# Optimization experiments

Measured on AMD Instinct MI355X. Metric: run time of the kernel, lower is better.

## Reference

```python
import jax, jax.numpy as jnp
import numpy as np

N_TOPICS = 1024
TOPIC_DIM = 128
HIDDEN = 512
N_HEADS = 8
HEAD_DIM = HIDDEN // N_HEADS
N_LAYERS = 2
ALPHA = 0.2
TIME_DECAY = 0.1
BATCH = 8


def setup_inputs() -> dict:
    key = jax.random.key(0)
    ks = jax.random.split(key, 16)
    inp = {
        'topic_ids': jax.random.randint(ks[0], (BATCH,), 0, N_TOPICS, dtype=jnp.int32),
        'adj_matrix': jax.random.randint(ks[1], (BATCH, N_TOPICS, N_TOPICS), 0, 2, dtype=jnp.int32),
        'time_matrix': jax.random.uniform(ks[2], (BATCH, N_TOPICS, N_TOPICS), dtype=jnp.float32),
        'attractiveness': jax.random.normal(ks[3], (BATCH,), dtype=jnp.float32),
        # parameters (torch Linear convention: W [out,in], y = x@W.T + b)
        'topic_embedding': jax.random.normal(ks[4], (N_TOPICS, TOPIC_DIM), dtype=jnp.float32) * 0.1,
        'struct_W': jax.random.normal(ks[5], (HIDDEN, TOPIC_DIM), dtype=jnp.float32) * 0.05,
        'struct_b': jnp.zeros((HIDDEN,), dtype=jnp.float32),
        'attract_W': jax.random.normal(ks[6], (HIDDEN, 1), dtype=jnp.float32) * 0.05,
        'attract_b': jnp.zeros((HIDDEN,), dtype=jnp.float32),
        'gat_W': jax.random.normal(ks[7], (N_LAYERS, N_HEADS, HIDDEN, HEAD_DIM), dtype=jnp.float32) * 0.05,
        'gat_a': jax.random.normal(ks[8], (N_LAYERS, N_HEADS, 2 * HEAD_DIM, 1), dtype=jnp.float32) * 0.05,
        'fc1_W': jax.random.normal(ks[9], (HIDDEN, HIDDEN), dtype=jnp.float32) * 0.05,
        'fc1_b': jnp.zeros((HIDDEN,), dtype=jnp.float32),
        'fc2_W': jax.random.normal(ks[10], (1, HIDDEN), dtype=jnp.float32) * 0.05,
        'fc2_b': jnp.zeros((1,), dtype=jnp.float32),
    }
    return inp


def _gat_layer(node, adj, time_w, W, a):
    # node: [B,N,F], adj: [B,N,N] (0/1), time_w: [B,N,N]
    # W: [H,F,hd], a: [H,2*hd,1]
    h = jnp.einsum('bni,hio->bhno', node, W)  # [B,H,N,hd]
    # Additive attention: a = [a_src; a_dst] so e_ij = LeakyReLU(h_i.a_src + h_j.a_dst)
    a_src = a[:, :HEAD_DIM, 0]   # [H,hd]
    a_dst = a[:, HEAD_DIM:, 0]   # [H,hd]
    e_src = jnp.einsum('bhnd,hd->bhn', h, a_src)  # [B,H,N]
    e_dst = jnp.einsum('bhnd,hd->bhn', h, a_dst)  # [B,H,N]
    e = e_src[:, :, :, None] + e_dst[:, :, None, :]  # [B,H,N,N]
    e = jax.nn.leaky_relu(e, negative_slope=ALPHA)
    e = e * time_w[:, None, :, :]
    e = jnp.where(adj[:, None, :, :] == 0, -jnp.inf, e)
    attn = jax.nn.softmax(e, axis=-1)
    out = jnp.einsum('bhij,bhjd->bhid', attn, h)  # [B,H,N,hd]
    out = out.transpose(0, 2, 1, 3).reshape(node.shape[0], node.shape[1], -1)
    return jax.nn.elu(out)


def reference(topic_ids, adj_matrix, time_matrix, attractiveness,
              topic_embedding, struct_W, struct_b, attract_W, attract_b,
              gat_W, gat_a, fc1_W, fc1_b, fc2_W, fc2_b):
    # structural features for all topics -> hidden
    struct = topic_embedding @ struct_W.T + struct_b          # [N,hidden]
    attract = attractiveness[:, None] @ attract_W.T + attract_b  # [B,hidden]
    node = jnp.broadcast_to(struct[None], (BATCH, N_TOPICS, HIDDEN))
    # weighted co-occurrence time (eq.17)
    time_w = jnp.exp(-TIME_DECAY * (time_matrix.max() - time_matrix))  # [B,N,N]
    for l in range(N_LAYERS):
        node = _gat_layer(node, adj_matrix, time_w, gat_W[l], gat_a[l])
    # gather per-sample topic node feature
    topic_feat = jnp.take_along_axis(node, topic_ids[:, None, None].astype(jnp.int32), axis=1)[:, 0]  # [B,hidden]
    combined = topic_feat + attract
    hidden = jax.nn.relu(combined @ fc1_W.T + fc1_b)
    pred = hidden @ fc2_W.T + fc2_b  # [B,1]
    return pred
```

## Files before the change

kernel.cpp:

```cpp
#include <hip/hip_runtime.h>

#define NT 1024
#define TD 128
#define HID 512
#define NH 8
#define HD 64
#define NB 8

typedef unsigned short us;
typedef short bf16x8 __attribute__((ext_vector_type(8)));
typedef float f32x4 __attribute__((ext_vector_type(4)));

#define LOG2E 1.44269504f

__device__ __forceinline__ us f2bf(float x) {
    unsigned int u = __float_as_uint(x);
    return (us)((u + 0x7FFFu + ((u >> 16) & 1u)) >> 16);
}
__device__ __forceinline__ float bf2f(us s) {
    return __uint_as_float(((unsigned int)s) << 16);
}

__global__ __launch_bounds__(256) void kprep(const float* __restrict__ tm, float* __restrict__ part,
                                             const float* __restrict__ emb, const float* __restrict__ sW,
// ... 18 lines not shown
    } else if (bx < 1152) {
        int g = bx - 1024; int iblk = g & 15, oseg = g >> 4;
        us* As = (us*)smf;
        us* Bs = (us*)smf + 64 * 136;
        const float4* esrc = (const float4*)(emb + (size_t)iblk * 64 * TD);
        const float4* wsrc = (const float4*)(sW + (size_t)oseg * 64 * TD);
        #pragma unroll
        for (int rep = 0; rep < 8; rep++) {
            int f = rep * 256 + t;
            int row = f >> 5, c4 = f & 31;
            float4 av = esrc[f];
            float4 bv = wsrc[f];
            us pa[4] = {f2bf(av.x), f2bf(av.y), f2bf(av.z), f2bf(av.w)};
            us pb[4] = {f2bf(bv.x), f2bf(bv.y), f2bf(bv.z), f2bf(bv.w)};
            *(uint2*)&As[row * 136 + c4 * 4] = *(uint2*)pa;
            *(uint2*)&Bs[row * 136 + c4 * 4] = *(uint2*)pb;
        }
        __syncthreads();
        int l = t & 63, w = t >> 6, m = l & 15, q = l >> 4;
        f32x4 acc[4];
        #pragma unroll
        for (int ot = 0; ot < 4; ot++) acc[ot] = (f32x4){0.f, 0.f, 0.f, 0.f};
        #pragma unroll
        for (int ks = 0; ks < 4; ks++) {
            bf16x8 a = *(const bf16x8*)&As[(w * 16 + m) * 136 + ks * 32 + q * 8];
            #pragma unroll
            for (int ot = 0; ot < 4; ot++) {
                bf16x8 b = *(const bf16x8*)&Bs[(ot * 16 + m) * 136 + ks * 32 + q * 8];
                acc[ot] = __builtin_amdgcn_mfma_f32_16x16x32_bf16(a, b, acc[ot], 0, 0, 0);
            }
        }
        #pragma unroll
        for (int ot = 0; ot < 4; ot++) {
            int col = oseg * 64 + ot * 16 + m;
            float sbv = sb[col];
            #pragma unroll
            for (int rr = 0; rr < 4; rr++) {
                int rowi = iblk * 64 + w * 16 + q * 4 + rr;
                node0b[(size_t)rowi * HID + col] = f2bf(acc[ot][rr] + sbv);
            }
        }
    } else if (bx < 1280) {
        int g = bx - 1152; int lh = g >> 3, kt = g & 7;
        float* tile = smf;
        const float4* src = (const float4*)(gW + ((size_t)lh * HID + kt * 64) * HD);
        #pragma unroll
        for (int rep = 0; rep < 4; rep++) {
            int f = rep * 256 + t;
            float4 v = src[f];
            int row = f >> 4, col = (f & 15) * 4;
            float* d = tile + row * 65 + col;
            d[0] = v.x; d[1] = v.y; d[2] = v.z; d[3] = v.w;
        }
        __syncthreads();
        int o = t >> 2, ks = (t & 3) * 16;
        us pk[16];
        #pragma unroll
        for (int j = 0; j < 16; j++) pk[j] = f2bf(tile[(ks + j) * 65 + o]);
        us* dst = Wt + (size_t)lh * HD * HID + (size_t)o * HID + kt * 64 + ks;
        *(uint4*)dst = *(uint4*)pk;
        *(uint4*)(dst + 8) = *(uint4*)&pk[8];
    } else {
        int hp = bx - 1280;
        if (hp == 0 && t < NB) out[t] = fc2b[0];
        const float* gsrc = ga + (size_t)(NH + hp) * 2 * HD;
        const float* wbase = gW + (size_t)(NH + hp) * HID * HD;
        #pragma unroll
        for (int rep = 0; rep < 2; rep++) {
            int k = rep * 256 + t;
            const float* wr = wbase + (size_t)k * HD;
            float s = 0.f, d = 0.f;
            #pragma unroll 8
            for (int o = 0; o < HD; o++) {
                float wv = wr[o];
                s = fmaf(wv, gsrc[o], s);
                d = fmaf(wv, gsrc[HD + o], d);
            }
            ws2[hp * HID + k] = s;
            ws2[(8 + hp) * HID + k] = d;
        }
    }
}

__device__ __forceinline__ void gemm_body(const us* __restrict__ A, const us* __restrict__ W,
                                          const float* __restrict__ gav,
                                          us* __restrict__ outT,
                                          float* __restrict__ esO, float* __restrict__ edO,
                                          int iblk, int b, int h, int t, us* sm) {
    us* As = sm;
    us* Bs = sm + 2 * 4608;
    int row = t >> 2, ks = t & 3;
    int l = t & 63, w = t >> 6, m = l & 15, q = l >> 4;
    size_t arow0 = (size_t)(b * NT + iblk * 64);
    const us* ar = A + (arow0 + row) * HID + ks * 16;
    const us* br = W + ((size_t)(h * HD + row)) * HID + ks * 16;
    f32x4 acc[4];
    #pragma unroll
    for (int ot = 0; ot < 4; ot++) acc[ot] = (f32x4){0.f, 0.f, 0.f, 0.f};
    {
        uint4 x0 = *(const uint4*)ar, x1 = *(const uint4*)(ar + 8);
        uint4 y0 = *(const uint4*)br, y1 = *(const uint4*)(br + 8);
        *(uint4*)&As[row * 72 + ks * 16] = x0; *(uint4*)&As[row * 72 + ks * 16 + 8] = x1;
        *(uint4*)&Bs[row * 72 + ks * 16] = y0; *(uint4*)&Bs[row * 72 + ks * 16 + 8] = y1;
    }
    uint4 a0 = *(const uint4*)(ar + 64), a1 = *(const uint4*)(ar + 72);
    uint4 b0 = *(const uint4*)(br + 64), b1 = *(const uint4*)(br + 72);
    for (int it = 0; it < 8; it++) {
        int cur = it & 1, nxt = cur ^ 1;
        uint4 na0, na1, nb0, nb1;
        if (it < 6) {
            int k0 = (it + 2) * 64;
            na0 = *(const uint4*)(ar + k0); na1 = *(const uint4*)(ar + k0 + 8);
            nb0 = *(const uint4*)(br + k0); nb1 = *(const uint4*)(br + k0 + 8);
        }
        __syncthreads();
        if (it < 7) {
            *(uint4*)&As[nxt * 4608 + row * 72 + ks * 16] = a0;
            *(uint4*)&As[nxt * 4608 + row * 72 + ks * 16 + 8] = a1;
            *(uint4*)&Bs[nxt * 4608 + row * 72 + ks * 16] = b0;
            *(uint4*)&Bs[nxt * 4608 + row * 72 + ks * 16 + 8] = b1;
        }
        const us* Ac = As + cur * 4608; const us* Bc = Bs + cur * 4608;
        #pragma unroll
        for (int kt = 0; kt < 2; kt++) {
            bf16x8 av = *(const bf16x8*)&Ac[(w * 16 + m) * 72 + kt * 32 + q * 8];
            #pragma unroll
            for (int ot = 0; ot < 4; ot++) {
                bf16x8 bv = *(const bf16x8*)&Bc[(ot * 16 + m) * 72 + kt * 32 + q * 8];
                acc[ot] = __builtin_amdgcn_mfma_f32_16x16x32_bf16(av, bv, acc[ot], 0, 0, 0);
            }
        }
        if (it < 6) { a0 = na0; a1 = na1; b0 = nb0; b1 = nb1; }
    }
    const float* gas = gav + h * 2 * HD;
    float gs[4], gd[4];
    #pragma unroll
    for (int ot = 0; ot < 4; ot++) { gs[ot] = gas[ot * 16 + m]; gd[ot] = gas[HD + ot * 16 + m]; }
    size_t ebase = ((size_t)b * NH + h) * NT + iblk * 64;
    #pragma unroll
    for (int rr = 0; rr < 4; rr++) {
        float s = 0.f, d = 0.f;
        #pragma unroll
        for (int ot = 0; ot < 4; ot++) { float v = acc[ot][rr]; s = fmaf(v, gs[ot], s); d = fmaf(v, gd[ot], d); }
        #pragma unroll
        for (int mask = 1; mask < 16; mask <<= 1) { s += __shfl_xor(s, mask); d += __shfl_xor(d, mask); }
        if (m == 0) {
            int rowi = w * 16 + q * 4 + rr;
            esO[ebase + rowi] = s;
            edO[ebase + rowi] = d;
        }
    }
    #pragma unroll
    for (int ot = 0; ot < 4; ot++) {
        int col = h * HD + ot * 16 + m;
        #pragma unroll
        for (int rr = 0; rr < 4; rr++) {
            int i_loc = w * 16 + q * 4 + rr;
            outT[(size_t)col * NT + iblk * 64 + i_loc] = f2bf(acc[ot][rr]);
        }
    }
}

#define ZF4 33808
__global__ __launch_bounds__(256) void kphase1(const float* __restrict__ tm, const int* __restrict__ adj,
                                               const float* __restrict__ part, us* __restrict__ TWb,
                                               const us* __restrict__ node0b, const us* __restrict__ Wt,
                                               const float* __restrict__ ga, us* __restrict__ Ht1,
                                               float* __restrict__ es1, float* __restrict__ ed1,
                                               float* __restrict__ zbase) {
    __shared__ __align__(16) us sm[4 * 4608];
    int bx = blockIdx.x, t = threadIdx.x;
    if (bx < 2048) {
        float* red = (float*)sm;
        float m = fmaxf(fmaxf(part[t * 4], part[t * 4 + 1]), fmaxf(part[t * 4 + 2], part[t * 4 + 3]));
        red[t] = m; __syncthreads();
        for (int s = 128; s > 0; s >>= 1) { if (t < s) red[t] = fmaxf(red[t], red[t + s]); __syncthreads(); }
        float tmx = red[0];
        const float C = 0.1f * LOG2E;
        #pragma unroll
        for (int it = 0; it < 4; it++) {
            size_t idx = (((size_t)bx * 4 + it) * 256 + t) * 4;
            float4 tv = *(const float4*)(tm + idx);
            int4 av = *(const int4*)(adj + idx);
            float w0 = exp2f((tv.x - tmx) * C) * LOG2E;
            float w1 = exp2f((tv.y - tmx) * C) * LOG2E;
            float w2 = exp2f((tv.z - tmx) * C) * LOG2E;
            float w3 = exp2f((tv.w - tmx) * C) * LOG2E;
            unsigned int fa = av.x ? __float_as_uint(w0) : 0x7FC00000u;
            unsigned int fb = av.y ? __float_as_uint(w1) : 0x7FC00000u;
            unsigned int fc = av.z ? __float_as_uint(w2) : 0x7FC00000u;
            unsigned int fd = av.w ? __float_as_uint(w3) : 0x7FC00000u;
            uint2 pk;
            pk.x = __builtin_amdgcn_perm(fb, fa, 0x07060302);
            pk.y = __builtin_amdgcn_perm(fd, fc, 0x07060302);
            *(uint2*)&TWb[idx] = pk;
        }
    } else if (bx < 2176) {
        int g = bx - 2048;
        gemm_body(node0b, Wt, ga, Ht1, es1, ed1, g & 15, 0, g >> 4, t, sm);
    } else {
        size_t idx = (size_t)(bx - 2176) * 256 + t;
        if (idx < ZF4) ((float4*)zbase)[idx] = (float4){0.f, 0.f, 0.f, 0.f};
    }
}

__global__ __launch_bounds__(256) void kedge(const float* __restrict__ es, const float* __restrict__ ed,
                                             us* __restrict__ E1) {
    int g = blockIdx.x;
    int h = g >> 8, i0 = (g & 255) << 2;
    int t = threadIdx.x;
    __shared__ float eds[NT];
    *(float4*)&eds[t * 4] = *(const float4*)&ed[h * NT + t * 4];
    __syncthreads();
    int j = t * 4;
    float4 e4 = *(const float4*)&eds[j];
    #pragma unroll
    for (int r = 0; r < 4; r++) {
        float esv = es[h * NT + i0 + r];
        float a = esv + e4.x; a = fmaxf(a, 0.2f * a);
        float bq = esv + e4.y; bq = fmaxf(bq, 0.2f * bq);
        float c = esv + e4.z; c = fmaxf(c, 0.2f * c);
        float d = esv + e4.w; d = fmaxf(d, 0.2f * d);
        uint2 pk;
        pk.x = __builtin_amdgcn_perm(__float_as_uint(bq), __float_as_uint(a), 0x07060302);
        pk.y = __builtin_amdgcn_perm(__float_as_uint(d), __float_as_uint(c), 0x07060302);
        *(uint2*)&E1[((size_t)(h * NT) + i0 + r) * NT + j] = pk;
    }
}

__device__ __forceinline__ void compute_p(uint4 T0, uint4 T1, uint4 E0, uint4 E1v,
                                          uint4& P01, uint4& P23) {
    union U { uint4 v; unsigned int w[4]; };
    U t0; t0.v = T0; U t1; t1.v = T1; U e0; e0.v = E0; U e1; e1.v = E1v;
    unsigned int pk[8];
    #pragma unroll
    for (int r = 0; r < 4; r++) {
        float twa = __uint_as_float(t0.w[r] << 16);
        float twb = __uint_as_float(t0.w[r] & 0xFFFF0000u);
        float Ea  = __uint_as_float(e0.w[r] << 16);
        float Eb  = __uint_as_float(e0.w[r] & 0xFFFF0000u);
        float pa = fmaxf(exp2f(twa * Ea), 0.f);
        float pb = fmaxf(exp2f(twb * Eb), 0.f);
        pk[r] = __builtin_amdgcn_perm(__float_as_uint(pb), __float_as_uint(pa), 0x07060302);
    }
    #pragma unroll
    for (int r = 0; r < 4; r++) {
        float twa = __uint_as_float(t1.w[r] << 16);
        float twb = __uint_as_float(t1.w[r] & 0xFFFF0000u);
        float Ea  = __uint_as_float(e1.w[r] << 16);
        float Eb  = __uint_as_float(e1.w[r] & 0xFFFF0000u);
        float pa = fmaxf(exp2f(twa * Ea), 0.f);
        float pb = fmaxf(exp2f(twb * Eb), 0.f);
        pk[4 + r] = __builtin_amdgcn_perm(__float_as_uint(pb), __float_as_uint(pa), 0x07060302);
    }
    P01 = make_uint4(pk[0], pk[1], pk[2], pk[3]);
    P23 = make_uint4(pk[4], pk[5], pk[6], pk[7]);
}

__global__ __launch_bounds__(256) void kattn1(const us* __restrict__ TWb, const us* __restrict__ Ht,
                                              const us* __restrict__ E1, const float* __restrict__ ws2,
                                              us* __restrict__ node1b,
                                              float* __restrict__ es2, float* __restrict__ ed2) {
    int x = blockIdx.x; int iblk = x & 15; int b = x >> 4; int h = blockIdx.y;
    int t = threadIdx.x;
    __shared__ __align__(16) us Ps[2 * 4608];
    __shared__ __align__(16) us Hs[2 * 4608];
    __shared__ float invl_s[64];
    int i = t >> 2, js = t & 3;
    int l = t & 63, w = t >> 6, m = l & 15, q = l >> 4;
    const us* twrow = TWb + ((size_t)(b * NT) + iblk * 64 + i) * NT + js * 16;
    const us* erow  = E1 + ((size_t)(h * NT) + iblk * 64 + i) * NT + js * 16;
    const us* htrow = Ht + ((size_t)(h * HD) + i) * NT + js * 16;
    f32x4 acc[4];
    #pragma unroll
    for (int ot = 0; ot < 4; ot++) acc[ot] = (f32x4){0.f, 0.f, 0.f, 0.f};
    f32x4 acc1 = (f32x4){0.f, 0.f, 0.f, 0.f};
    short ov = (m == 0) ? (short)0x3F80 : (short)0;
    bf16x8 bones = {ov, ov, ov, ov, ov, ov, ov, ov};
    uint4 T0, T1, E0, E1r, Hh0, Hh1;
    T0 = *(const uint4*)twrow; T1 = *(const uint4*)(twrow + 8);
    E0 = *(const uint4*)erow;  E1r = *(const uint4*)(erow + 8);
    Hh0 = *(const uint4*)htrow; Hh1 = *(const uint4*)(htrow + 8);
    {
        uint4 p01, p23;
        compute_p(T0, T1, E0, E1r, p01, p23);
        us* Pd = Ps + i * 72 + js * 16;
        us* Hd = Hs + i * 72 + js * 16;
        *(uint4*)Pd = p01; *(uint4*)(Pd + 8) = p23;
        *(uint4*)Hd = Hh0; *(uint4*)(Hd + 8) = Hh1;
    }
    T0 = *(const uint4*)(twrow + 64); T1 = *(const uint4*)(twrow + 72);
    E0 = *(const uint4*)(erow + 64);  E1r = *(const uint4*)(erow + 72);
    Hh0 = *(const uint4*)(htrow + 64); Hh1 = *(const uint4*)(htrow + 72);
    for (int it = 0; it < 16; it++) {
        int cur = it & 1, nxt = cur ^ 1;
        uint4 nT0, nT1, nE0, nE1, nH0, nH1;
        if (it < 14) {
            int j0 = (it + 2) * 64;
            nT0 = *(const uint4*)(twrow + j0); nT1 = *(const uint4*)(twrow + j0 + 8);
            nE0 = *(const uint4*)(erow + j0);  nE1 = *(const uint4*)(erow + j0 + 8);
            nH0 = *(const uint4*)(htrow + j0); nH1 = *(const uint4*)(htrow + j0 + 8);
        }
        uint4 p01, p23;
        if (it < 15) compute_p(T0, T1, E0, E1r, p01, p23);
        __syncthreads();
        if (it < 15) {
            us* Pd = Ps + nxt * 4608 + i * 72 + js * 16;
            us* Hd = Hs + nxt * 4608 + i * 72 + js * 16;
            *(uint4*)Pd = p01; *(uint4*)(Pd + 8) = p23;
            *(uint4*)Hd = Hh0; *(uint4*)(Hd + 8) = Hh1;
        }
        const us* Pc = Ps + cur * 4608; const us* Hc = Hs + cur * 4608;
        #pragma unroll
        for (int kt = 0; kt < 2; kt++) {
            bf16x8 av = *(const bf16x8*)&Pc[(w * 16 + m) * 72 + kt * 32 + q * 8];
            #pragma unroll
            for (int ot = 0; ot < 4; ot++) {
                bf16x8 bv = *(const bf16x8*)&Hc[(ot * 16 + m) * 72 + kt * 32 + q * 8];
                acc[ot] = __builtin_amdgcn_mfma_f32_16x16x32_bf16(av, bv, acc[ot], 0, 0, 0);
            }
            acc1 = __builtin_amdgcn_mfma_f32_16x16x32_bf16(av, bones, acc1, 0, 0, 0);
        }
        if (it < 14) { T0 = nT0; T1 = nT1; E0 = nE0; E1r = nE1; Hh0 = nH0; Hh1 = nH1; }
    }
    if (m == 0) {
        #pragma unroll
        for (int rr = 0; rr < 4; rr++) invl_s[w * 16 + q * 4 + rr] = 1.f / acc1[rr];
    }
    __syncthreads();
    float varr[4][4];
    #pragma unroll
    for (int ot = 0; ot < 4; ot++) {
        int col = h * HD + ot * 16 + m;
        #pragma unroll
        for (int rr = 0; rr < 4; rr++) {
            int i_loc = w * 16 + q * 4 + rr;
            float v = acc[ot][rr] * invl_s[i_loc];
            v = v > 0.f ? v : (__expf(v) - 1.f);
            varr[ot][rr] = v;
            node1b[(size_t)(b * NT + iblk * 64 + i_loc) * HID + col] = f2bf(v);
        }
    }
    #pragma unroll
    for (int h2 = 0; h2 < NH; h2++) {
        float wsv[4], wdv[4];
        #pragma unroll
        for (int ot = 0; ot < 4; ot++) {
            int col = h * HD + ot * 16 + m;
            wsv[ot] = ws2[h2 * HID + col];
            wdv[ot] = ws2[(8 + h2) * HID + col];
        }
        #pragma unroll
        for (int rr = 0; rr < 4; rr++) {
            float s = 0.f, d = 0.f;
            #pragma unroll
            for (int ot = 0; ot < 4; ot++) { s = fmaf(varr[ot][rr], wsv[ot], s); d = fmaf(varr[ot][rr], wdv[ot], d); }
            #pragma unroll
            for (int mask = 1; mask < 16; mask <<= 1) { s += __shfl_xor(s, mask); d += __shfl_xor(d, mask); }
            if (m == 0) {
                int ig = iblk * 64 + w * 16 + q * 4 + rr;
                atomicAdd(&es2[(size_t)(b * NH + h2) * NT + ig], s);
                atomicAdd(&ed2[(size_t)(b * NH + h2) * NT + ig], d);
            }
        }
    }
}

__global__ __launch_bounds__(256) void kgemm2(const us* __restrict__ node1b, const us* __restrict__ Wt2,
                                              const us* __restrict__ TWb,
                                              const float* __restrict__ es2, const float* __restrict__ ed2,
                                              const int* __restrict__ topic_ids,
                                              float* __restrict__ pv, float* __restrict__ pl) {
    __shared__ __align__(16) us sm[4 * 4608];
    __shared__ float pv_s[4][64];
    __shared__ float pl_s[4];
    int x = blockIdx.x; int iblk = x & 15; int b = x >> 4; int h = blockIdx.y;
    int t = threadIdx.x;
    us* As = sm;
    us* Bs = sm + 2 * 4608;
    int row = t >> 2, ks = t & 3;
    int l = t & 63, w = t >> 6, m = l & 15, q = l >> 4;
    size_t arow0 = (size_t)(b * NT + iblk * 64);
    const us* ar = node1b + (arow0 + row) * HID + ks * 16;
    const us* br = Wt2 + ((size_t)(h * HD + row)) * HID + ks * 16;
    f32x4 acc[4];
    #pragma unroll
    for (int ot = 0; ot < 4; ot++) acc[ot] = (f32x4){0.f, 0.f, 0.f, 0.f};
    {
        uint4 x0 = *(const uint4*)ar, x1 = *(const uint4*)(ar + 8);
        uint4 y0 = *(const uint4*)br, y1 = *(const uint4*)(br + 8);
        *(uint4*)&As[row * 72 + ks * 16] = x0; *(uint4*)&As[row * 72 + ks * 16 + 8] = x1;
        *(uint4*)&Bs[row * 72 + ks * 16] = y0; *(uint4*)&Bs[row * 72 + ks * 16 + 8] = y1;
    }
    uint4 a0 = *(const uint4*)(ar + 64), a1 = *(const uint4*)(ar + 72);
    uint4 b0 = *(const uint4*)(br + 64), b1 = *(const uint4*)(br + 72);
    for (int it = 0; it < 8; it++) {
        int cur = it & 1, nxt = cur ^ 1;
        uint4 na0, na1, nb0, nb1;
        if (it < 6) {
            int k0 = (it + 2) * 64;
            na0 = *(const uint4*)(ar + k0); na1 = *(const uint4*)(ar + k0 + 8);
            nb0 = *(const uint4*)(br + k0); nb1 = *(const uint4*)(br + k0 + 8);
        }
        __syncthreads();
        if (it < 7) {
            *(uint4*)&As[nxt * 4608 + row * 72 + ks * 16] = a0;
            *(uint4*)&As[nxt * 4608 + row * 72 + ks * 16 + 8] = a1;
            *(uint4*)&Bs[nxt * 4608 + row * 72 + ks * 16] = b0;
            *(uint4*)&Bs[nxt * 4608 + row * 72 + ks * 16 + 8] = b1;
        }
        const us* Ac = As + cur * 4608; const us* Bc = Bs + cur * 4608;
        #pragma unroll
        for (int kt = 0; kt < 2; kt++) {
            bf16x8 av = *(const bf16x8*)&Ac[(w * 16 + m) * 72 + kt * 32 + q * 8];
            #pragma unroll
            for (int ot = 0; ot < 4; ot++) {
                bf16x8 bv = *(const bf16x8*)&Bc[(ot * 16 + m) * 72 + kt * 32 + q * 8];
                acc[ot] = __builtin_amdgcn_mfma_f32_16x16x32_bf16(av, bv, acc[ot], 0, 0, 0);
            }
        }
        if (it < 6) { a0 = na0; a1 = na1; b0 = nb0; b1 = nb1; }
    }
    int qi = topic_ids[b];
    float es_q = es2[(size_t)(b * NH + h) * NT + qi];
    float pvp[4] = {0.f, 0.f, 0.f, 0.f};
    float psum = 0.f;
    #pragma unroll
    for (int rr = 0; rr < 4; rr++) {
        int j = iblk * 64 + w * 16 + q * 4 + rr;
        float edj = ed2[(size_t)(b * NH + h) * NT + j];
        float tw = bf2f(TWb[((size_t)(b * NT) + qi) * NT + j]);
        float e = es_q + edj;
        e = fmaxf(e, 0.2f * e) * tw;
        float pj = fmaxf(exp2f(e), 0.f);
        psum += pj;
        #pragma unroll
        for (int ot = 0; ot < 4; ot++) pvp[ot] = fmaf(pj, acc[ot][rr], pvp[ot]);
    }
    #pragma unroll
    for (int mask = 16; mask < 64; mask <<= 1) {
        psum += __shfl_xor(psum, mask);
        #pragma unroll
        for (int ot = 0; ot < 4; ot++) pvp[ot] += __shfl_xor(pvp[ot], mask);
    }
    if (q == 0) {
        #pragma unroll
        for (int ot = 0; ot < 4; ot++) pv_s[w][ot * 16 + m] = pvp[ot];
        if (m == 0) pl_s[w] = psum;
    }
    __syncthreads();
    if (t < 64) {
        float s = pv_s[0][t] + pv_s[1][t] + pv_s[2][t] + pv_s[3][t];
        atomicAdd(&pv[(size_t)(b * NH + h) * HD + t], s);
    }
    if (t == 0) atomicAdd(&pl[b * NH + h], pl_s[0] + pl_s[1] + pl_s[2] + pl_s[3]);
}

__global__ __launch_bounds__(256) void khead2(const float* __restrict__ pv, const float* __restrict__ pl,
                                              const float* __restrict__ attr,
                                              const float* __restrict__ aW, const float* __restrict__ ab,
                                              const float* __restrict__ fc1W, const float* __restrict__ fc1b,
                                              const float* __restrict__ fc2W, float* __restrict__ out) {
    int kseg = blockIdx.x, b = blockIdx.y;
    int t = threadIdx.x;
    __shared__ float comb[HID];
    __shared__ float linv[NH];
    __shared__ float r2[256];
    if (t < NH) linv[t] = 1.f / pl[b * NH + t];
    __syncthreads();
    float av = attr[b];
    for (int k = t; k < HID; k += 256) {
        int h = k >> 6, o = k & 63;
        float v = pv[(size_t)(b * NH + h) * HD + o] * linv[h];
        v = v > 0.f ? v : (__expf(v) - 1.f);
        comb[k] = v + av * aW[k] + ab[k];
    }
    __syncthreads();
    int kk = kseg * 16 + (t >> 4);
    int j = t & 15;
    const float* row = fc1W + (size_t)kk * HID;
    float acc = 0.f;
    #pragma unroll 8
    for (int mi = 0; mi < 32; mi++) {
        int idx = mi * 16 + j;
        acc = fmaf(comb[idx], row[idx], acc);
    }
    #pragma unroll
    for (int mask = 1; mask < 16; mask <<= 1) acc += __shfl_xor(acc, mask);
    float partv = 0.f;
    if (j == 0) {
        float hk = fmaxf(acc + fc1b[kk], 0.f);
        partv = hk * fc2W[kk];
    }
    r2[t] = partv; __syncthreads();
    for (int s = 128; s > 0; s >>= 1) { if (t < s) r2[t] += r2[t + s]; __syncthreads(); }
    if (t == 0) atomicAdd(&out[b], r2[0]);
}

extern "C" void kernel_launch(void* const* d_in, const int* in_sizes, int n_in,
                              void* d_out, int out_size, void* d_ws, size_t ws_size,
                              hipStream_t stream) {
    const int*   topic_ids = (const int*)d_in[0];
    const int*   adj       = (const int*)d_in[1];
    const float* tm        = (const float*)d_in[2];
    const float* attr      = (const float*)d_in[3];
    const float* emb       = (const float*)d_in[4];
    const float* sW        = (const float*)d_in[5];
    const float* sb        = (const float*)d_in[6];
    const float* aW        = (const float*)d_in[7];
    const float* ab        = (const float*)d_in[8];
    const float* gW        = (const float*)d_in[9];
    const float* ga        = (const float*)d_in[10];
    const float* fc1W      = (const float*)d_in[11];
    const float* fc1b      = (const float*)d_in[12];
    const float* fc2W      = (const float*)d_in[13];
    const float* fc2b      = (const float*)d_in[14];
    float* out = (float*)d_out;

    char* p = (char*)d_ws;
    us* TWb    = (us*)p; p += sizeof(us) * (size_t)NB * NT * NT;
    us* E1     = (us*)p; p += sizeof(us) * (size_t)NH * NT * NT;
    us* node0b = (us*)p; p += sizeof(us) * (size_t)NT * HID;
    us* Wt     = (us*)p; p += sizeof(us) * (size_t)2 * NH * HD * HID;
    us* Ht1    = (us*)p; p += sizeof(us) * (size_t)HID * NT;
    us* node1b = (us*)p; p += sizeof(us) * (size_t)NB * NT * HID;
    float* es1  = (float*)p; p += sizeof(float) * NH * NT;
    float* ed1  = (float*)p; p += sizeof(float) * NH * NT;
    float* es2  = (float*)p; p += sizeof(float) * NB * NH * NT;
    float* ed2  = (float*)p; p += sizeof(float) * NB * NH * NT;
    float* pv   = (float*)p; p += sizeof(float) * NB * NH * HD;
    float* pl   = (float*)p; p += sizeof(float) * NB * NH;
    float* ws2  = (float*)p; p += sizeof(float) * 16 * HID;
    float* part = (float*)p; p += sizeof(float) * 1024;

    kprep<<<1288, 256, 0, stream>>>(tm, part, emb, sW, sb, node0b, gW, Wt, ga, ws2, fc2b, out);
    kphase1<<<2309, 256, 0, stream>>>(tm, adj, part, TWb, node0b, Wt, ga, Ht1, es1, ed1, es2);
    kedge<<<2048, 256, 0, stream>>>(es1, ed1, E1);
    kattn1<<<dim3(16 * NB, NH), 256, 0, stream>>>(TWb, Ht1, E1, ws2, node1b, es2, ed2);
    kgemm2<<<dim3(16 * NB, NH), 256, 0, stream>>>(node1b, Wt + (size_t)NH * HD * HID, TWb,
                                                  es2, ed2, topic_ids, pv, pl);
    khead2<<<dim3(32, NB), 256, 0, stream>>>(pv, pl, attr, aW, ab, fc1W, fc1b, fc2W, out);
}
```

Baseline: 211.9 us.

## Drop LDS staging in GEMMs and compute only query-row layer-2 scores

The three MFMA loops (layer-1 projection, attention aggregation, layer-2 projection) now load operands straight from global memory into registers in the MFMA fragment layout. This removes the shared-memory double buffers and barriers. Layer-2 source scores are now computed only for the queried topic row, and destination scores are computed inline in kgemm2 from its accumulators. That removes the full es2/ed2 buffers, their per-row atomic updates and the large zero-fill. The cost is less reuse of global loads within a block, so more traffic goes through L2, and unaligned 16-byte row loads may coalesce less well.

```diff
diff --git a/kernel.cpp b/kernel.cpp
--- a/kernel.cpp
+++ b/kernel.cpp
@@ -124,61 +124,28 @@
     }
 }
 
-__device__ __forceinline__ void gemm_body(const us* __restrict__ A, const us* __restrict__ W,
-                                          const float* __restrict__ gav,
-                                          us* __restrict__ outT,
-                                          float* __restrict__ esO, float* __restrict__ edO,
-                                          int iblk, int b, int h, int t, us* sm) {
-    us* As = sm;
-    us* Bs = sm + 2 * 4608;
-    int row = t >> 2, ks = t & 3;
+__device__ __forceinline__ void gemm1_body(const us* __restrict__ A, const us* __restrict__ W,
+                                           const float* __restrict__ gav, us* __restrict__ outT,
+                                           float* __restrict__ esO, float* __restrict__ edO,
+                                           int iblk, int h, int t) {
     int l = t & 63, w = t >> 6, m = l & 15, q = l >> 4;
-    size_t arow0 = (size_t)(b * NT + iblk * 64);
-    const us* ar = A + (arow0 + row) * HID + ks * 16;
-    const us* br = W + ((size_t)(h * HD + row)) * HID + ks * 16;
+    const us* ar = A + ((size_t)(iblk * 64 + w * 16 + m)) * HID + q * 8;
+    const us* br = W + ((size_t)(h * HD) + m) * HID + q * 8;
     f32x4 acc[4];
     #pragma unroll
     for (int ot = 0; ot < 4; ot++) acc[ot] = (f32x4){0.f, 0.f, 0.f, 0.f};
-    {
-        uint4 x0 = *(const uint4*)ar, x1 = *(const uint4*)(ar + 8);
-        uint4 y0 = *(const uint4*)br, y1 = *(const uint4*)(br + 8);
-        *(uint4*)&As[row * 72 + ks * 16] = x0; *(uint4*)&As[row * 72 + ks * 16 + 8] = x1;
-        *(uint4*)&Bs[row * 72 + ks * 16] = y0; *(uint4*)&Bs[row * 72 + ks * 16 + 8] = y1;
-    }
-    uint4 a0 = *(const uint4*)(ar + 64), a1 = *(const uint4*)(ar + 72);
-    uint4 b0 = *(const uint4*)(br + 64), b1 = *(const uint4*)(br + 72);
-    for (int it = 0; it < 8; it++) {
-        int cur = it & 1, nxt = cur ^ 1;
-        uint4 na0, na1, nb0, nb1;
-        if (it < 6) {
-            int k0 = (it + 2) * 64;
-            na0 = *(const uint4*)(ar + k0); na1 = *(const uint4*)(ar + k0 + 8);
-            nb0 = *(const uint4*)(br + k0); nb1 = *(const uint4*)(br + k0 + 8);
-        }
-        __syncthreads();
-        if (it < 7) {
-            *(uint4*)&As[nxt * 4608 + row * 72 + ks * 16] = a0;
-            *(uint4*)&As[nxt * 4608 + row * 72 + ks * 16 + 8] = a1;
-            *(uint4*)&Bs[nxt * 4608 + row * 72 + ks * 16] = b0;
-            *(uint4*)&Bs[nxt * 4608 + row * 72 + ks * 16 + 8] = b1;
-        }
-        const us* Ac = As + cur * 4608; const us* Bc = Bs + cur * 4608;
-        #pragma unroll
-        for (int kt = 0; kt < 2; kt++) {
-            bf16x8 av = *(const bf16x8*)&Ac[(w * 16 + m) * 72 + kt * 32 + q * 8];
-            #pragma unroll
-            for (int ot = 0; ot < 4; ot++) {
-                bf16x8 bv = *(const bf16x8*)&Bc[(ot * 16 + m) * 72 + kt * 32 + q * 8];
-                acc[ot] = __builtin_amdgcn_mfma_f32_16x16x32_bf16(av, bv, acc[ot], 0, 0, 0);
-            }
-        }
-        if (it < 6) { a0 = na0; a1 = na1; b0 = nb0; b1 = nb1; }
+    #pragma unroll 4
+    for (int k0 = 0; k0 < HID; k0 += 32) {
+        bf16x8 a = *(const bf16x8*)(ar + k0);
+        acc[0] = __builtin_amdgcn_mfma_f32_16x16x32_bf16(a, *(const bf16x8*)(br + k0), acc[0], 0, 0, 0);
+        acc[1] = __builtin_amdgcn_mfma_f32_16x16x32_bf16(a, *(const bf16x8*)(br + 16 * HID + k0), acc[1], 0, 0, 0);
+        acc[2] = __builtin_amdgcn_mfma_f32_16x16x32_bf16(a, *(const bf16x8*)(br + 32 * HID + k0), acc[2], 0, 0, 0);
+        acc[3] = __builtin_amdgcn_mfma_f32_16x16x32_bf16(a, *(const bf16x8*)(br + 48 * HID + k0), acc[3], 0, 0, 0);
     }
     const float* gas = gav + h * 2 * HD;
     float gs[4], gd[4];
     #pragma unroll
     for (int ot = 0; ot < 4; ot++) { gs[ot] = gas[ot * 16 + m]; gd[ot] = gas[HD + ot * 16 + m]; }
-    size_t ebase = ((size_t)b * NH + h) * NT + iblk * 64;
     #pragma unroll
     for (int rr = 0; rr < 4; rr++) {
         float s = 0.f, d = 0.f;
@@ -187,9 +154,9 @@
         #pragma unroll
         for (int mask = 1; mask < 16; mask <<= 1) { s += __shfl_xor(s, mask); d += __shfl_xor(d, mask); }
         if (m == 0) {
-            int rowi = w * 16 + q * 4 + rr;
-            esO[ebase + rowi] = s;
-            edO[ebase + rowi] = d;
+            int rowi = iblk * 64 + w * 16 + q * 4 + rr;
+            esO[h * NT + rowi] = s;
+            edO[h * NT + rowi] = d;
         }
     }
     #pragma unroll
@@ -197,23 +164,22 @@
         int col = h * HD + ot * 16 + m;
         #pragma unroll
         for (int rr = 0; rr < 4; rr++) {
-            int i_loc = w * 16 + q * 4 + rr;
-            outT[(size_t)col * NT + iblk * 64 + i_loc] = f2bf(acc[ot][rr]);
-        }
-    }
-}
-
-#define ZF4 33808
+            int i_loc = iblk * 64 + w * 16 + q * 4 + rr;
+            outT[(size_t)col * NT + i_loc] = f2bf(acc[ot][rr]);
+        }
+    }
+}
+
+#define ZF4 1056
 __global__ __launch_bounds__(256) void kphase1(const float* __restrict__ tm, const int* __restrict__ adj,
                                                const float* __restrict__ part, us* __restrict__ TWb,
                                                const us* __restrict__ node0b, const us* __restrict__ Wt,
                                                const float* __restrict__ ga, us* __restrict__ Ht1,
                                                float* __restrict__ es1, float* __restrict__ ed1,
                                                float* __restrict__ zbase) {
-    __shared__ __align__(16) us sm[4 * 4608];
     int bx = blockIdx.x, t = threadIdx.x;
     if (bx < 2048) {
-        float* red = (float*)sm;
+        __shared__ float red[256];
         float m = fmaxf(fmaxf(part[t * 4], part[t * 4 + 1]), fmaxf(part[t * 4 + 2], part[t * 4 + 3]));
         red[t] = m; __syncthreads();
         for (int s = 128; s > 0; s >>= 1) { if (t < s) red[t] = fmaxf(red[t], red[t + s]); __syncthreads(); }
@@ -239,9 +205,9 @@
         }
     } else if (bx < 2176) {
         int g = bx - 2048;
-        gemm_body(node0b, Wt, ga, Ht1, es1, ed1, g & 15, 0, g >> 4, t, sm);
+        gemm1_body(node0b, Wt, ga, Ht1, es1, ed1, g & 15, g >> 4, t);
     } else {
-        size_t idx = (size_t)(bx - 2176) * 256 + t;
+        int idx = (bx - 2176) * 256 + t;
         if (idx < ZF4) ((float4*)zbase)[idx] = (float4){0.f, 0.f, 0.f, 0.f};
     }
 }
@@ -270,100 +236,57 @@
     }
 }
 
-__device__ __forceinline__ void compute_p(uint4 T0, uint4 T1, uint4 E0, uint4 E1v,
-                                          uint4& P01, uint4& P23) {
-    union U { uint4 v; unsigned int w[4]; };
-    U t0; t0.v = T0; U t1; t1.v = T1; U e0; e0.v = E0; U e1; e1.v = E1v;
-    unsigned int pk[8];
+__device__ __forceinline__ bf16x8 compute_p8(uint4 T, uint4 E) {
+    union { uint4 v; unsigned int w[4]; } tu, eu;
+    tu.v = T; eu.v = E;
+    unsigned int pk[4];
     #pragma unroll
     for (int r = 0; r < 4; r++) {
-        float twa = __uint_as_float(t0.w[r] << 16);
-        float twb = __uint_as_float(t0.w[r] & 0xFFFF0000u);
-        float Ea  = __uint_as_float(e0.w[r] << 16);
-        float Eb  = __uint_as_float(e0.w[r] & 0xFFFF0000u);
+        float twa = __uint_as_float(tu.w[r] << 16);
+        float twb = __uint_as_float(tu.w[r] & 0xFFFF0000u);
+        float Ea  = __uint_as_float(eu.w[r] << 16);
+        float Eb  = __uint_as_float(eu.w[r] & 0xFFFF0000u);
         float pa = fmaxf(exp2f(twa * Ea), 0.f);
         float pb = fmaxf(exp2f(twb * Eb), 0.f);
         pk[r] = __builtin_amdgcn_perm(__float_as_uint(pb), __float_as_uint(pa), 0x07060302);
     }
-    #pragma unroll
-    for (int r = 0; r < 4; r++) {
-        float twa = __uint_as_float(t1.w[r] << 16);
-        float twb = __uint_as_float(t1.w[r] & 0xFFFF0000u);
-        float Ea  = __uint_as_float(e1.w[r] << 16);
-        float Eb  = __uint_as_float(e1.w[r] & 0xFFFF0000u);
-        float pa = fmaxf(exp2f(twa * Ea), 0.f);
-        float pb = fmaxf(exp2f(twb * Eb), 0.f);
-        pk[4 + r] = __builtin_amdgcn_perm(__float_as_uint(pb), __float_as_uint(pa), 0x07060302);
-    }
-    P01 = make_uint4(pk[0], pk[1], pk[2], pk[3]);
-    P23 = make_uint4(pk[4], pk[5], pk[6], pk[7]);
+    union { uint4 v; bf16x8 b; } o;
+    o.v = make_uint4(pk[0], pk[1], pk[2], pk[3]);
+    return o.b;
 }
 
 __global__ __launch_bounds__(256) void kattn1(const us* __restrict__ TWb, const us* __restrict__ Ht,
                                               const us* __restrict__ E1, const float* __restrict__ ws2,
-                                              us* __restrict__ node1b,
-                                              float* __restrict__ es2, float* __restrict__ ed2) {
+                                              const int* __restrict__ topic_ids,
+                                              us* __restrict__ node1b, float* __restrict__ es2q) {
     int x = blockIdx.x; int iblk = x & 15; int b = x >> 4; int h = blockIdx.y;
     int t = threadIdx.x;
-    __shared__ __align__(16) us Ps[2 * 4608];
-    __shared__ __align__(16) us Hs[2 * 4608];
+    int l = t & 63, w = t >> 6, m = l & 15, q = l >> 4;
     __shared__ float invl_s[64];
-    int i = t >> 2, js = t & 3;
-    int l = t & 63, w = t >> 6, m = l & 15, q = l >> 4;
-    const us* twrow = TWb + ((size_t)(b * NT) + iblk * 64 + i) * NT + js * 16;
-    const us* erow  = E1 + ((size_t)(h * NT) + iblk * 64 + i) * NT + js * 16;
-    const us* htrow = Ht + ((size_t)(h * HD) + i) * NT + js * 16;
+    int ia = iblk * 64 + w * 16 + m;
+    const us* twrow = TWb + ((size_t)(b * NT) + ia) * NT + q * 8;
+    const us* erow  = E1 + ((size_t)(h * NT) + ia) * NT + q * 8;
+    const us* htrow = Ht + ((size_t)(h * HD) + m) * NT + q * 8;
     f32x4 acc[4];
     #pragma unroll
     for (int ot = 0; ot < 4; ot++) acc[ot] = (f32x4){0.f, 0.f, 0.f, 0.f};
     f32x4 acc1 = (f32x4){0.f, 0.f, 0.f, 0.f};
     short ov = (m == 0) ? (short)0x3F80 : (short)0;
     bf16x8 bones = {ov, ov, ov, ov, ov, ov, ov, ov};
-    uint4 T0, T1, E0, E1r, Hh0, Hh1;
-    T0 = *(const uint4*)twrow; T1 = *(const uint4*)(twrow + 8);
-    E0 = *(const uint4*)erow;  E1r = *(const uint4*)(erow + 8);
-    Hh0 = *(const uint4*)htrow; Hh1 = *(const uint4*)(htrow + 8);
-    {
-        uint4 p01, p23;
-        compute_p(T0, T1, E0, E1r, p01, p23);
-        us* Pd = Ps + i * 72 + js * 16;
-        us* Hd = Hs + i * 72 + js * 16;
-        *(uint4*)Pd = p01; *(uint4*)(Pd + 8) = p23;
-        *(uint4*)Hd = Hh0; *(uint4*)(Hd + 8) = Hh1;
-    }
-    T0 = *(const uint4*)(twrow + 64); T1 = *(const uint4*)(twrow + 72);
-    E0 = *(const uint4*)(erow + 64);  E1r = *(const uint4*)(erow + 72);
-    Hh0 = *(const uint4*)(htrow + 64); Hh1 = *(const uint4*)(htrow + 72);
-    for (int it = 0; it < 16; it++) {
-        int cur = it & 1, nxt = cur ^ 1;
-        uint4 nT0, nT1, nE0, nE1, nH0, nH1;
-        if (it < 14) {
-            int j0 = (it + 2) * 64;
-            nT0 = *(const uint4*)(twrow + j0); nT1 = *(const uint4*)(twrow + j0 + 8);
-            nE0 = *(const uint4*)(erow + j0);  nE1 = *(const uint4*)(erow + j0 + 8);
-            nH0 = *(const uint4*)(htrow + j0); nH1 = *(const uint4*)(htrow + j0 + 8);
-        }
-        uint4 p01, p23;
-        if (it < 15) compute_p(T0, T1, E0, E1r, p01, p23);
-        __syncthreads();
-        if (it < 15) {
-            us* Pd = Ps + nxt * 4608 + i * 72 + js * 16;
-            us* Hd = Hs + nxt * 4608 + i * 72 + js * 16;
-            *(uint4*)Pd = p01; *(uint4*)(Pd + 8) = p23;
-            *(uint4*)Hd = Hh0; *(uint4*)(Hd + 8) = Hh1;
-        }
-        const us* Pc = Ps + cur * 4608; const us* Hc = Hs + cur * 4608;
-        #pragma unroll
-        for (int kt = 0; kt < 2; kt++) {
-            bf16x8 av = *(const bf16x8*)&Pc[(w * 16 + m) * 72 + kt * 32 + q * 8];
-            #pragma unroll
-            for (int ot = 0; ot < 4; ot++) {
-                bf16x8 bv = *(const bf16x8*)&Hc[(ot * 16 + m) * 72 + kt * 32 + q * 8];
-                acc[ot] = __builtin_amdgcn_mfma_f32_16x16x32_bf16(av, bv, acc[ot], 0, 0, 0);
-            }
-            acc1 = __builtin_amdgcn_mfma_f32_16x16x32_bf16(av, bones, acc1, 0, 0, 0);
-        }
-        if (it < 14) { T0 = nT0; T1 = nT1; E0 = nE0; E1r = nE1; Hh0 = nH0; Hh1 = nH1; }
+    #pragma unroll 2
+    for (int j0 = 0; j0 < NT; j0 += 32) {
+        uint4 T = *(const uint4*)(twrow + j0);
+        uint4 E = *(const uint4*)(erow + j0);
+        bf16x8 b0 = *(const bf16x8*)(htrow + j0);
+        bf16x8 b1 = *(const bf16x8*)(htrow + 16 * NT + j0);
+        bf16x8 b2 = *(const bf16x8*)(htrow + 32 * NT + j0);
+        bf16x8 b3 = *(const bf16x8*)(htrow + 48 * NT + j0);
+        bf16x8 a = compute_p8(T, E);
+        acc[0] = __builtin_amdgcn_mfma_f32_16x16x32_bf16(a, b0, acc[0], 0, 0, 0);
+        acc[1] = __builtin_amdgcn_mfma_f32_16x16x32_bf16(a, b1, acc[1], 0, 0, 0);
+        acc[2] = __builtin_amdgcn_mfma_f32_16x16x32_bf16(a, b2, acc[2], 0, 0, 0);
+        acc[3] = __builtin_amdgcn_mfma_f32_16x16x32_bf16(a, b3, acc[3], 0, 0, 0);
+        acc1   = __builtin_amdgcn_mfma_f32_16x16x32_bf16(a, bones, acc1, 0, 0, 0);
     }
     if (m == 0) {
         #pragma unroll
@@ -383,96 +306,63 @@
             node1b[(size_t)(b * NT + iblk * 64 + i_loc) * HID + col] = f2bf(v);
         }
     }
-    #pragma unroll
-    for (int h2 = 0; h2 < NH; h2++) {
-        float wsv[4], wdv[4];
-        #pragma unroll
-        for (int ot = 0; ot < 4; ot++) {
-            int col = h * HD + ot * 16 + m;
-            wsv[ot] = ws2[h2 * HID + col];
-            wdv[ot] = ws2[(8 + h2) * HID + col];
-        }
-        #pragma unroll
-        for (int rr = 0; rr < 4; rr++) {
-            float s = 0.f, d = 0.f;
+    int qi = topic_ids[b];
+    if ((qi >> 6) == iblk && w == ((qi & 63) >> 4) && q == ((qi >> 2) & 3)) {
+        int rr = qi & 3;
+        #pragma unroll
+        for (int h2 = 0; h2 < NH; h2++) {
+            float s = 0.f;
             #pragma unroll
-            for (int ot = 0; ot < 4; ot++) { s = fmaf(varr[ot][rr], wsv[ot], s); d = fmaf(varr[ot][rr], wdv[ot], d); }
+            for (int ot = 0; ot < 4; ot++)
+                s = fmaf(varr[ot][rr], ws2[h2 * HID + h * HD + ot * 16 + m], s);
             #pragma unroll
-            for (int mask = 1; mask < 16; mask <<= 1) { s += __shfl_xor(s, mask); d += __shfl_xor(d, mask); }
-            if (m == 0) {
-                int ig = iblk * 64 + w * 16 + q * 4 + rr;
-                atomicAdd(&es2[(size_t)(b * NH + h2) * NT + ig], s);
-                atomicAdd(&ed2[(size_t)(b * NH + h2) * NT + ig], d);
-            }
+            for (int mask = 1; mask < 16; mask <<= 1) s += __shfl_xor(s, mask);
+            if (m == 0) atomicAdd(&es2q[b * NH + h2], s);
         }
     }
 }
 
 __global__ __launch_bounds__(256) void kgemm2(const us* __restrict__ node1b, const us* __restrict__ Wt2,
-                                              const us* __restrict__ TWb,
-                                              const float* __restrict__ es2, const float* __restrict__ ed2,
+                                              const us* __restrict__ TWb, const float* __restrict__ ga2,
+                                              const float* __restrict__ es2q,
                                               const int* __restrict__ topic_ids,
                                               float* __restrict__ pv, float* __restrict__ pl) {
-    __shared__ __align__(16) us sm[4 * 4608];
+    int x = blockIdx.x; int iblk = x & 15; int b = x >> 4; int h = blockIdx.y;
+    int t = threadIdx.x;
+    int l = t & 63, w = t >> 6, m = l & 15, q = l >> 4;
     __shared__ float pv_s[4][64];
     __shared__ float pl_s[4];
-    int x = blockIdx.x; int iblk = x & 15; int b = x >> 4; int h = blockIdx.y;
-    int t = threadIdx.x;
-    us* As = sm;
-    us* Bs = sm + 2 * 4608;
-    int row = t >> 2, ks = t & 3;
-    int l = t & 63, w = t >> 6, m = l & 15, q = l >> 4;
-    size_t arow0 = (size_t)(b * NT + iblk * 64);
-    const us* ar = node1b + (arow0 + row) * HID + ks * 16;
-    const us* br = Wt2 + ((size_t)(h * HD + row)) * HID + ks * 16;
+    const us* ar = node1b + ((size_t)(b * NT) + iblk * 64 + w * 16 + m) * HID + q * 8;
+    const us* br = Wt2 + ((size_t)(h * HD) + m) * HID + q * 8;
     f32x4 acc[4];
     #pragma unroll
     for (int ot = 0; ot < 4; ot++) acc[ot] = (f32x4){0.f, 0.f, 0.f, 0.f};
-    {
-        uint4 x0 = *(const uint4*)ar, x1 = *(const uint4*)(ar + 8);
-        uint4 y0 = *(const uint4*)br, y1 = *(const uint4*)(br + 8);
-        *(uint4*)&As[row * 72 + ks * 16] = x0; *(uint4*)&As[row * 72 + ks * 16 + 8] = x1;
-        *(uint4*)&Bs[row * 72 + ks * 16] = y0; *(uint4*)&Bs[row * 72 + ks * 16 + 8] = y1;
-    }
-    uint4 a0 = *(const uint4*)(ar + 64), a1 = *(const uint4*)(ar + 72);
-    uint4 b0 = *(const uint4*)(br + 64), b1 = *(const uint4*)(br + 72);
-    for (int it = 0; it < 8; it++) {
-        int cur = it & 1, nxt = cur ^ 1;
-        uint4 na0, na1, nb0, nb1;
-        if (it < 6) {
-            int k0 = (it + 2) * 64;
-            na0 = *(const uint4*)(ar + k0); na1 = *(const uint4*)(ar + k0 + 8);
-            nb0 = *(const uint4*)(br + k0); nb1 = *(const uint4*)(br + k0 + 8);
-        }
-        __syncthreads();
-        if (it < 7) {
-            *(uint4*)&As[nxt * 4608 + row * 72 + ks * 16] = a0;
-            *(uint4*)&As[nxt * 4608 + row * 72 + ks * 16 + 8] = a1;
-            *(uint4*)&Bs[nxt * 4608 + row * 72 + ks * 16] = b0;
-            *(uint4*)&Bs[nxt * 4608 + row * 72 + ks * 16 + 8] = b1;
-        }
-        const us* Ac = As + cur * 4608; const us* Bc = Bs + cur * 4608;
-        #pragma unroll
-        for (int kt = 0; kt < 2; kt++) {
-            bf16x8 av = *(const bf16x8*)&Ac[(w * 16 + m) * 72 + kt * 32 + q * 8];
-            #pragma unroll
-            for (int ot = 0; ot < 4; ot++) {
-                bf16x8 bv = *(const bf16x8*)&Bc[(ot * 16 + m) * 72 + kt * 32 + q * 8];
-                acc[ot] = __builtin_amdgcn_mfma_f32_16x16x32_bf16(av, bv, acc[ot], 0, 0, 0);
-            }
-        }
-        if (it < 6) { a0 = na0; a1 = na1; b0 = nb0; b1 = nb1; }
+    #pragma unroll 4
+    for (int k0 = 0; k0 < HID; k0 += 32) {
+        bf16x8 a = *(const bf16x8*)(ar + k0);
+        acc[0] = __builtin_amdgcn_mfma_f32_16x16x32_bf16(a, *(const bf16x8*)(br + k0), acc[0], 0, 0, 0);
+        acc[1] = __builtin_amdgcn_mfma_f32_16x16x32_bf16(a, *(const bf16x8*)(br + 16 * HID + k0), acc[1], 0, 0, 0);
+        acc[2] = __builtin_amdgcn_mfma_f32_16x16x32_bf16(a, *(const bf16x8*)(br + 32 * HID + k0), acc[2], 0, 0, 0);
+        acc[3] = __builtin_amdgcn_mfma_f32_16x16x32_bf16(a, *(const bf16x8*)(br + 48 * HID + k0), acc[3], 0, 0, 0);
     }
     int qi = topic_ids[b];
-    float es_q = es2[(size_t)(b * NH + h) * NT + qi];
+    float es_q = es2q[b * NH + h];
+    const float* gad = ga2 + h * 2 * HD + HD;
+    float gd[4];
+    #pragma unroll
+    for (int ot = 0; ot < 4; ot++) gd[ot] = gad[ot * 16 + m];
     float pvp[4] = {0.f, 0.f, 0.f, 0.f};
     float psum = 0.f;
     #pragma unroll
     for (int rr = 0; rr < 4; rr++) {
+        float d = 0.f;
+        #pragma unroll
+        for (int ot = 0; ot < 4; ot++) d = fmaf(acc[ot][rr], gd[ot], d);
+        #pragma unroll
+        for (int mask = 1; mask < 16; mask <<= 1) d += __shfl_xor(d, mask);
         int j = iblk * 64 + w * 16 + q * 4 + rr;
-        float edj = ed2[(size_t)(b * NH + h) * NT + j];
         float tw = bf2f(TWb[((size_t)(b * NT) + qi) * NT + j]);
-        float e = es_q + edj;
+        float e = es_q + d;
         e = fmaxf(e, 0.2f * e) * tw;
         float pj = fmaxf(exp2f(e), 0.f);
         psum += pj;
@@ -568,18 +458,17 @@
     us* node1b = (us*)p; p += sizeof(us) * (size_t)NB * NT * HID;
     float* es1  = (float*)p; p += sizeof(float) * NH * NT;
     float* ed1  = (float*)p; p += sizeof(float) * NH * NT;
-    float* es2  = (float*)p; p += sizeof(float) * NB * NH * NT;
-    float* ed2  = (float*)p; p += sizeof(float) * NB * NH * NT;
+    float* es2q = (float*)p; p += sizeof(float) * NB * NH;
     float* pv   = (float*)p; p += sizeof(float) * NB * NH * HD;
     float* pl   = (float*)p; p += sizeof(float) * NB * NH;
     float* ws2  = (float*)p; p += sizeof(float) * 16 * HID;
     float* part = (float*)p; p += sizeof(float) * 1024;
 
     kprep<<<1288, 256, 0, stream>>>(tm, part, emb, sW, sb, node0b, gW, Wt, ga, ws2, fc2b, out);
-    kphase1<<<2309, 256, 0, stream>>>(tm, adj, part, TWb, node0b, Wt, ga, Ht1, es1, ed1, es2);
+    kphase1<<<2181, 256, 0, stream>>>(tm, adj, part, TWb, node0b, Wt, ga, Ht1, es1, ed1, es2q);
     kedge<<<2048, 256, 0, stream>>>(es1, ed1, E1);
-    kattn1<<<dim3(16 * NB, NH), 256, 0, stream>>>(TWb, Ht1, E1, ws2, node1b, es2, ed2);
+    kattn1<<<dim3(16 * NB, NH), 256, 0, stream>>>(TWb, Ht1, E1, ws2, topic_ids, node1b, es2q);
     kgemm2<<<dim3(16 * NB, NH), 256, 0, stream>>>(node1b, Wt + (size_t)NH * HD * HID, TWb,
-                                                  es2, ed2, topic_ids, pv, pl);
+                                                  ga + NH * 2 * HD, es2q, topic_ids, pv, pl);
     khead2<<<dim3(32, NB), 256, 0, stream>>>(pv, pl, attr, aW, ab, fc1W, fc1b, fc2W, out);
 }
```

After: 292.0 us. 37.8% more time.

## Compute layer-2 attention source score only for query row, dst score in GEMM epilogue

Applied to the files above, without the earlier changes.

Layer-2 source scores are now computed only for the queried topic row per batch via a single guarded atomic path in kattn1, rather than for all nodes with many atomics. Destination scores are computed directly from the layer-2 GEMM accumulators in kgemm2's epilogue using the attention vector, removing the full es2/ed2 arrays and their zeroing. This cuts atomic traffic, the zero-fill work and global reads, at the cost of extra shuffles in kgemm2. Only the query row's output is needed, so this is legitimate work elimination.

```diff
diff --git a/kernel.cpp b/kernel.cpp
--- a/kernel.cpp
+++ b/kernel.cpp
@@ -124,17 +124,15 @@
     }
 }
 
-__device__ __forceinline__ void gemm_body(const us* __restrict__ A, const us* __restrict__ W,
-                                          const float* __restrict__ gav,
-                                          us* __restrict__ outT,
-                                          float* __restrict__ esO, float* __restrict__ edO,
-                                          int iblk, int b, int h, int t, us* sm) {
+__device__ __forceinline__ void gemm1_body(const us* __restrict__ A, const us* __restrict__ W,
+                                           const float* __restrict__ gav, us* __restrict__ outT,
+                                           float* __restrict__ esO, float* __restrict__ edO,
+                                           int iblk, int h, int t, us* sm) {
     us* As = sm;
     us* Bs = sm + 2 * 4608;
     int row = t >> 2, ks = t & 3;
     int l = t & 63, w = t >> 6, m = l & 15, q = l >> 4;
-    size_t arow0 = (size_t)(b * NT + iblk * 64);
-    const us* ar = A + (arow0 + row) * HID + ks * 16;
+    const us* ar = A + ((size_t)(iblk * 64 + row)) * HID + ks * 16;
     const us* br = W + ((size_t)(h * HD + row)) * HID + ks * 16;
     f32x4 acc[4];
     #pragma unroll
@@ -178,7 +176,6 @@
     float gs[4], gd[4];
     #pragma unroll
     for (int ot = 0; ot < 4; ot++) { gs[ot] = gas[ot * 16 + m]; gd[ot] = gas[HD + ot * 16 + m]; }
-    size_t ebase = ((size_t)b * NH + h) * NT + iblk * 64;
     #pragma unroll
     for (int rr = 0; rr < 4; rr++) {
         float s = 0.f, d = 0.f;
@@ -187,9 +184,9 @@
         #pragma unroll
         for (int mask = 1; mask < 16; mask <<= 1) { s += __shfl_xor(s, mask); d += __shfl_xor(d, mask); }
         if (m == 0) {
-            int rowi = w * 16 + q * 4 + rr;
-            esO[ebase + rowi] = s;
-            edO[ebase + rowi] = d;
+            int rowi = iblk * 64 + w * 16 + q * 4 + rr;
+            esO[h * NT + rowi] = s;
+            edO[h * NT + rowi] = d;
         }
     }
     #pragma unroll
@@ -197,13 +194,13 @@
         int col = h * HD + ot * 16 + m;
         #pragma unroll
         for (int rr = 0; rr < 4; rr++) {
-            int i_loc = w * 16 + q * 4 + rr;
-            outT[(size_t)col * NT + iblk * 64 + i_loc] = f2bf(acc[ot][rr]);
-        }
-    }
-}
-
-#define ZF4 33808
+            int i_loc = iblk * 64 + w * 16 + q * 4 + rr;
+            outT[(size_t)col * NT + i_loc] = f2bf(acc[ot][rr]);
+        }
+    }
+}
+
+#define ZF4 1056
 __global__ __launch_bounds__(256) void kphase1(const float* __restrict__ tm, const int* __restrict__ adj,
                                                const float* __restrict__ part, us* __restrict__ TWb,
                                                const us* __restrict__ node0b, const us* __restrict__ Wt,
@@ -239,9 +236,9 @@
         }
     } else if (bx < 2176) {
         int g = bx - 2048;
-        gemm_body(node0b, Wt, ga, Ht1, es1, ed1, g & 15, 0, g >> 4, t, sm);
+        gemm1_body(node0b, Wt, ga, Ht1, es1, ed1, g & 15, g >> 4, t, sm);
     } else {
-        size_t idx = (size_t)(bx - 2176) * 256 + t;
+        int idx = (bx - 2176) * 256 + t;
         if (idx < ZF4) ((float4*)zbase)[idx] = (float4){0.f, 0.f, 0.f, 0.f};
     }
 }
@@ -301,8 +298,8 @@
 
 __global__ __launch_bounds__(256) void kattn1(const us* __restrict__ TWb, const us* __restrict__ Ht,
                                               const us* __restrict__ E1, const float* __restrict__ ws2,
-                                              us* __restrict__ node1b,
-                                              float* __restrict__ es2, float* __restrict__ ed2) {
+                                              const int* __restrict__ topic_ids,
+                                              us* __restrict__ node1b, float* __restrict__ es2q) {
     int x = blockIdx.x; int iblk = x & 15; int b = x >> 4; int h = blockIdx.y;
     int t = threadIdx.x;
     __shared__ __align__(16) us Ps[2 * 4608];
@@ -383,34 +380,25 @@
             node1b[(size_t)(b * NT + iblk * 64 + i_loc) * HID + col] = f2bf(v);
         }
     }
-    #pragma unroll
-    for (int h2 = 0; h2 < NH; h2++) {
-        float wsv[4], wdv[4];
-        #pragma unroll
-        for (int ot = 0; ot < 4; ot++) {
-            int col = h * HD + ot * 16 + m;
-            wsv[ot] = ws2[h2 * HID + col];
-            wdv[ot] = ws2[(8 + h2) * HID + col];
-        }
-        #pragma unroll
-        for (int rr = 0; rr < 4; rr++) {
-            float s = 0.f, d = 0.f;
-            #pragma unroll
-            for (int ot = 0; ot < 4; ot++) { s = fmaf(varr[ot][rr], wsv[ot], s); d = fmaf(varr[ot][rr], wdv[ot], d); }
-            #pragma unroll
-            for (int mask = 1; mask < 16; mask <<= 1) { s += __shfl_xor(s, mask); d += __shfl_xor(d, mask); }
-            if (m == 0) {
-                int ig = iblk * 64 + w * 16 + q * 4 + rr;
-                atomicAdd(&es2[(size_t)(b * NH + h2) * NT + ig], s);
-                atomicAdd(&ed2[(size_t)(b * NH + h2) * NT + ig], d);
-            }
+    int qi = topic_ids[b];
+    if ((qi >> 6) == iblk && w == ((qi & 63) >> 4) && q == ((qi >> 2) & 3)) {
+        int rr = qi & 3;
+        #pragma unroll
+        for (int h2 = 0; h2 < NH; h2++) {
+            float s = 0.f;
+            #pragma unroll
+            for (int ot = 0; ot < 4; ot++)
+                s = fmaf(varr[ot][rr], ws2[h2 * HID + h * HD + ot * 16 + m], s);
+            #pragma unroll
+            for (int mask = 1; mask < 16; mask <<= 1) s += __shfl_xor(s, mask);
+            if (m == 0) atomicAdd(&es2q[b * NH + h2], s);
         }
     }
 }
 
 __global__ __launch_bounds__(256) void kgemm2(const us* __restrict__ node1b, const us* __restrict__ Wt2,
-                                              const us* __restrict__ TWb,
-                                              const float* __restrict__ es2, const float* __restrict__ ed2,
+                                              const us* __restrict__ TWb, const float* __restrict__ ga2,
+                                              const float* __restrict__ es2q,
                                               const int* __restrict__ topic_ids,
                                               float* __restrict__ pv, float* __restrict__ pl) {
     __shared__ __align__(16) us sm[4 * 4608];
@@ -422,8 +410,7 @@
     us* Bs = sm + 2 * 4608;
     int row = t >> 2, ks = t & 3;
     int l = t & 63, w = t >> 6, m = l & 15, q = l >> 4;
-    size_t arow0 = (size_t)(b * NT + iblk * 64);
-    const us* ar = node1b + (arow0 + row) * HID + ks * 16;
+    const us* ar = node1b + ((size_t)(b * NT) + iblk * 64 + row) * HID + ks * 16;
     const us* br = Wt2 + ((size_t)(h * HD + row)) * HID + ks * 16;
     f32x4 acc[4];
     #pragma unroll
@@ -464,15 +451,23 @@
         if (it < 6) { a0 = na0; a1 = na1; b0 = nb0; b1 = nb1; }
     }
     int qi = topic_ids[b];
-    float es_q = es2[(size_t)(b * NH + h) * NT + qi];
+    float es_q = es2q[b * NH + h];
+    const float* gad = ga2 + h * 2 * HD + HD;
+    float gd[4];
+    #pragma unroll
+    for (int ot = 0; ot < 4; ot++) gd[ot] = gad[ot * 16 + m];
     float pvp[4] = {0.f, 0.f, 0.f, 0.f};
     float psum = 0.f;
     #pragma unroll
     for (int rr = 0; rr < 4; rr++) {
+        float d = 0.f;
+        #pragma unroll
+        for (int ot = 0; ot < 4; ot++) d = fmaf(acc[ot][rr], gd[ot], d);
+        #pragma unroll
+        for (int mask = 1; mask < 16; mask <<= 1) d += __shfl_xor(d, mask);
         int j = iblk * 64 + w * 16 + q * 4 + rr;
-        float edj = ed2[(size_t)(b * NH + h) * NT + j];
         float tw = bf2f(TWb[((size_t)(b * NT) + qi) * NT + j]);
-        float e = es_q + edj;
+        float e = es_q + d;
         e = fmaxf(e, 0.2f * e) * tw;
         float pj = fmaxf(exp2f(e), 0.f);
         psum += pj;
@@ -568,18 +563,17 @@
     us* node1b = (us*)p; p += sizeof(us) * (size_t)NB * NT * HID;
     float* es1  = (float*)p; p += sizeof(float) * NH * NT;
     float* ed1  = (float*)p; p += sizeof(float) * NH * NT;
-    float* es2  = (float*)p; p += sizeof(float) * NB * NH * NT;
-    float* ed2  = (float*)p; p += sizeof(float) * NB * NH * NT;
+    float* es2q = (float*)p; p += sizeof(float) * NB * NH;
     float* pv   = (float*)p; p += sizeof(float) * NB * NH * HD;
     float* pl   = (float*)p; p += sizeof(float) * NB * NH;
     float* ws2  = (float*)p; p += sizeof(float) * 16 * HID;
     float* part = (float*)p; p += sizeof(float) * 1024;
 
     kprep<<<1288, 256, 0, stream>>>(tm, part, emb, sW, sb, node0b, gW, Wt, ga, ws2, fc2b, out);
-    kphase1<<<2309, 256, 0, stream>>>(tm, adj, part, TWb, node0b, Wt, ga, Ht1, es1, ed1, es2);
+    kphase1<<<2181, 256, 0, stream>>>(tm, adj, part, TWb, node0b, Wt, ga, Ht1, es1, ed1, es2q);
     kedge<<<2048, 256, 0, stream>>>(es1, ed1, E1);
-    kattn1<<<dim3(16 * NB, NH), 256, 0, stream>>>(TWb, Ht1, E1, ws2, node1b, es2, ed2);
+    kattn1<<<dim3(16 * NB, NH), 256, 0, stream>>>(TWb, Ht1, E1, ws2, topic_ids, node1b, es2q);
     kgemm2<<<dim3(16 * NB, NH), 256, 0, stream>>>(node1b, Wt + (size_t)NH * HD * HID, TWb,
-                                                  es2, ed2, topic_ids, pv, pl);
+                                                  ga + NH * 2 * HD, es2q, topic_ids, pv, pl);
     khead2<<<dim3(32, NB), 256, 0, stream>>>(pv, pl, attr, aW, ab, fc1W, fc1b, fc2W, out);
 }
```

After: 204.7 us. 3.4% less time.
